# Optimization experiments

Measured on AMD Instinct MI355X. Metric: run time of the kernel, lower is better.

## Reference

```python
import jax, jax.numpy as jnp
import numpy as np
from math import sqrt

B, C1, H1, W1 = 8, 256, 32, 32
C2, H2, W2 = 256, 32, 32
NH, KD, VD = 8, 64, 64


def setup_inputs() -> dict:
    key = jax.random.key(0)
    k = jax.random.split(key, 6)
    s = 0.02
    return {
        "input1": jax.random.normal(k[0], (B, C1, H1, W1), jnp.float32),
        "input2": jax.random.normal(k[1], (B, C2, H2, W2), jnp.float32),
        # torch nn.Linear weights are [out, in]; kept in that layout
        "Wk1": jax.random.normal(k[2], (KD * NH, C1), jnp.float32) * s,
        "Wk2": jax.random.normal(k[3], (KD * NH, C2), jnp.float32) * s,
        "Wv2": jax.random.normal(k[4], (VD * NH, C2), jnp.float32) * s,
        "Wo": jax.random.normal(k[5], (C1, VD * NH), jnp.float32) * s,
    }


def reference(input1, input2, Wk1, Wk2, Wv2, Wo):
    b, c1, h1, w1 = input1.shape
    _, c2, h2, w2 = input2.shape
    s1, s2 = h1 * w1, h2 * w2
    # [B, S, C]
    emb1 = input1.reshape(b, c1, s1).transpose(0, 2, 1)
    emb2 = input2.reshape(b, c2, s2).transpose(0, 2, 1)
    # projections -> [B, heads, S, d]
    k1 = (emb1 @ Wk1.T).reshape(b, s1, NH, KD).transpose(0, 2, 1, 3)
    k2 = (emb2 @ Wk2.T).reshape(b, s2, NH, KD).transpose(0, 2, 1, 3)
    v2 = (emb2 @ Wv2.T).reshape(b, s2, NH, VD).transpose(0, 2, 1, 3)
    # attention: [B, heads, S1, S2]
    scores = jnp.einsum("bhqd,bhkd->bhqk", k1, k2) / sqrt(KD)
    attn = jax.nn.softmax(scores, axis=-1)
    attn = jnp.nan_to_num(attn, nan=0.0)
    out = jnp.einsum("bhqk,bhkd->bhqd", attn, v2)  # [B, heads, S1, VD]
    out = out.transpose(0, 2, 1, 3).reshape(b, s1, NH * VD)
    out = out @ Wo.T  # [B, S1, C1]
    return out.transpose(0, 2, 1).reshape(b, c1, h1, w1)
```

## Files before the change

kernel.cpp:

```cpp
#include <hip/hip_runtime.h>
#include <stdint.h>

typedef __bf16 bf16_t;
typedef __attribute__((ext_vector_type(8))) __bf16 bf16x8;
typedef __attribute__((ext_vector_type(4))) __bf16 bf16x4;
typedef __attribute__((ext_vector_type(4))) float f32x4;

#define NB 8
#define NC 256
#define NS 1024
#define NHD 8
#define ND 64
#define NO 512

#define QK_SCALE 0.18033688011112042f

__device__ __forceinline__ f32x4 mfma16(bf16x8 a, bf16x8 b, f32x4 c) {
  return __builtin_amdgcn_mfma_f32_16x16x32_bf16(a, b, c, 0, 0, 0);
}

__device__ __forceinline__ void gll16(const bf16_t* g, const bf16_t* l) {
  auto gp = (const __attribute__((address_space(1))) void*)(uintptr_t)g;
  auto lp = (__attribute__((address_space(3))) void*)(uint32_t)(uintptr_t)l;
  __builtin_amdgcn_global_load_lds(gp, lp, 16, 0, 0);
}

__global__ __launch_bounds__(256) void k_tcvt(const float* __restrict__ x,
                                              bf16_t* __restrict__ xt) {
  __shared__ float tile[32][33];
  int b = blockIdx.z;
  int s0 = blockIdx.x * 32, c0 = blockIdx.y * 32;
  int tx = threadIdx.x, ty = threadIdx.y;
  const float* xb = x + (size_t)b * NC * NS;
#pragma unroll
  for (int i = 0; i < 4; ++i)
    tile[ty + 8 * i][tx] = xb[(size_t)(c0 + ty + 8 * i) * NS + s0 + tx];
  __syncthreads();
  bf16_t* xtb = xt + (size_t)b * NS * NC;
#pragma unroll
  for (int i = 0; i < 4; ++i)
    xtb[(size_t)(s0 + ty + 8 * i) * NC + c0 + tx] =
        (bf16_t)tile[tx][ty + 8 * i];
}

__global__ __launch_bounds__(256) void k_cvt4(
    const float* __restrict__ s0, const float* __restrict__ s1,
    const float* __restrict__ s2, const float* __restrict__ s3,
    bf16_t* __restrict__ d0, bf16_t* __restrict__ d1,
    bf16_t* __restrict__ d2, bf16_t* __restrict__ d3) {
  const float* s;
  bf16_t* d;
  switch (blockIdx.y) {
    case 0: s = s0; d = d0; break;
    case 1: s = s1; d = d1; break;
    case 2: s = s2; d = d2; break;
    default: s = s3; d = d3; break;
  }
  int i = (blockIdx.x * 256 + threadIdx.x) * 4;
  float4 v = *reinterpret_cast<const float4*>(s + i);
  bf16x4 o;
  o[0] = (bf16_t)v.x; o[1] = (bf16_t)v.y;
  o[2] = (bf16_t)v.z; o[3] = (bf16_t)v.w;
  *reinterpret_cast<bf16x4*>(d + i) = o;
}

__global__ __launch_bounds__(256) void k_projKs(const bf16_t* __restrict__ W,
                                                const bf16_t* __restrict__ XT,
                                                bf16_t* __restrict__ K,
                                                float scale) {
  __shared__ __align__(16) bf16_t lw[2][128 * 128];
  __shared__ __align__(16) bf16_t lx[2][128 * 128];
  int id = blockIdx.x;
  int b = id & 7;
  int ob = ((id >> 3) & 3) * 128;
  int sb = (id >> 5) * 128;
  int tid = threadIdx.x, wid = tid >> 6, lane = tid & 63;
  int lr = lane & 15, g = lane >> 4;
  const bf16_t* wsrc = W + (size_t)ob * NC;
  const bf16_t* xsrc = XT + ((size_t)b * NS + sb) * NC;

  int sr = tid >> 4, sc = tid & 15;
#pragma unroll
  for (int h = 0; h < 2; ++h)
#pragma unroll
    for (int it = 0; it < 8; ++it) {
      int row = it * 16 + sr;
      int cs = (sc & 8) | ((sc & 7) ^ (row & 7));
      gll16(wsrc + (size_t)row * NC + h * 128 + cs * 8,
            &lw[h][(it * 16 + wid * 4) * 128]);
      gll16(xsrc + (size_t)row * NC + h * 128 + cs * 8,
            &lx[h][(it * 16 + wid * 4) * 128]);
    }

  int o0 = (wid >> 1) * 64, s0 = (wid & 1) * 64;
  f32x4 acc[4][4];
#pragma unroll
  for (int mt = 0; mt < 4; ++mt)
#pragma unroll
    for (int nt = 0; nt < 4; ++nt) acc[mt][nt] = (f32x4){0.f, 0.f, 0.f, 0.f};

  asm volatile("s_waitcnt vmcnt(16)" ::: "memory");
  __builtin_amdgcn_s_barrier();
#pragma unroll
  for (int h = 0; h < 2; ++h) {
    if (h == 1) {
      asm volatile("s_waitcnt vmcnt(0)" ::: "memory");
      __builtin_amdgcn_s_barrier();
    }
#pragma unroll
    for (int kk = 0; kk < 4; ++kk) {
      int j = kk * 4 + g;
      bf16x8 av[4], bv[4];
#pragma unroll
      for (int mt = 0; mt < 4; ++mt) {
        int row = o0 + mt * 16 + lr;
        int jj = (j & 8) | ((j & 7) ^ (row & 7));
        av[mt] = *reinterpret_cast<const bf16x8*>(&lw[h][row * 128 + jj * 8]);
      }
#pragma unroll
      for (int nt = 0; nt < 4; ++nt) {
        int row = s0 + nt * 16 + lr;
        int jj = (j & 8) | ((j & 7) ^ (row & 7));
        bv[nt] = *reinterpret_cast<const bf16x8*>(&lx[h][row * 128 + jj * 8]);
      }
#pragma unroll
      for (int mt = 0; mt < 4; ++mt)
#pragma unroll
        for (int nt = 0; nt < 4; ++nt)
          acc[mt][nt] = mfma16(av[mt], bv[nt], acc[mt][nt]);
    }
  }
#pragma unroll
  for (int mt = 0; mt < 4; ++mt) {
    int oRow = ob + o0 + mt * 16 + g * 4;
    int hh = oRow >> 6, d0 = oRow & 63;
#pragma unroll
    for (int nt = 0; nt < 4; ++nt) {
      int s = sb + s0 + nt * 16 + lr;
      bf16x4 pk;
      pk[0] = (bf16_t)(acc[mt][nt][0] * scale);
      pk[1] = (bf16_t)(acc[mt][nt][1] * scale);
      pk[2] = (bf16_t)(acc[mt][nt][2] * scale);
      pk[3] = (bf16_t)(acc[mt][nt][3] * scale);
      *reinterpret_cast<bf16x4*>(
          K + (((size_t)b * NHD + hh) * NS + s) * ND + d0) = pk;
    }
  }
}

__global__ __launch_bounds__(256) void k_projVs(const bf16_t* __restrict__ Wv,
                                                const bf16_t* __restrict__ XT,
                                                bf16_t* __restrict__ VT) {
  __shared__ __align__(16) bf16_t lw[2][128 * 128];
  __shared__ __align__(16) bf16_t lx[2][128 * 128];
  int id = blockIdx.x;
  int b = id & 7;
  int ob = ((id >> 3) & 3) * 128;
  int sb = (id >> 5) * 128;
  int tid = threadIdx.x, wid = tid >> 6, lane = tid & 63;
  int lr = lane & 15, g = lane >> 4;
  const bf16_t* wsrc = Wv + (size_t)ob * NC;
  const bf16_t* xsrc = XT + ((size_t)b * NS + sb) * NC;

  int sr = tid >> 4, sc = tid & 15;
#pragma unroll
  for (int h = 0; h < 2; ++h)
#pragma unroll
    for (int it = 0; it < 8; ++it) {
      int row = it * 16 + sr;
      int cs = (sc & 8) | ((sc & 7) ^ (row & 7));
      gll16(wsrc + (size_t)row * NC + h * 128 + cs * 8,
            &lw[h][(it * 16 + wid * 4) * 128]);
      gll16(xsrc + (size_t)row * NC + h * 128 + cs * 8,
            &lx[h][(it * 16 + wid * 4) * 128]);
    }

  int s0 = (wid >> 1) * 64, o0 = (wid & 1) * 64;
  f32x4 acc[4][4];
#pragma unroll
  for (int mt = 0; mt < 4; ++mt)
#pragma unroll
    for (int nt = 0; nt < 4; ++nt) acc[mt][nt] = (f32x4){0.f, 0.f, 0.f, 0.f};

  asm volatile("s_waitcnt vmcnt(16)" ::: "memory");
  __builtin_amdgcn_s_barrier();
#pragma unroll
  for (int h = 0; h < 2; ++h) {
    if (h == 1) {
      asm volatile("s_waitcnt vmcnt(0)" ::: "memory");
      __builtin_amdgcn_s_barrier();
    }
#pragma unroll
    for (int kk = 0; kk < 4; ++kk) {
      int j = kk * 4 + g;
      bf16x8 av[4], bv[4];
#pragma unroll
      for (int mt = 0; mt < 4; ++mt) {
        int row = s0 + mt * 16 + lr;
        int jj = (j & 8) | ((j & 7) ^ (row & 7));
        av[mt] = *reinterpret_cast<const bf16x8*>(&lx[h][row * 128 + jj * 8]);
      }
#pragma unroll
      for (int nt = 0; nt < 4; ++nt) {
        int row = o0 + nt * 16 + lr;
        int jj = (j & 8) | ((j & 7) ^ (row & 7));
        bv[nt] = *reinterpret_cast<const bf16x8*>(&lw[h][row * 128 + jj * 8]);
      }
#pragma unroll
      for (int mt = 0; mt < 4; ++mt)
#pragma unroll
        for (int nt = 0; nt < 4; ++nt)
          acc[mt][nt] = mfma16(av[mt], bv[nt], acc[mt][nt]);
    }
  }
#pragma unroll
  for (int mt = 0; mt < 4; ++mt) {
    int sRow = sb + s0 + mt * 16 + g * 4;
#pragma unroll
    for (int nt = 0; nt < 4; ++nt) {
      int o = ob + o0 + nt * 16 + lr;
      int hh = o >> 6, d = o & 63;
      bf16x4 pk;
      pk[0] = (bf16_t)acc[mt][nt][0];
      pk[1] = (bf16_t)acc[mt][nt][1];
      pk[2] = (bf16_t)acc[mt][nt][2];
      pk[3] = (bf16_t)acc[mt][nt][3];
      *reinterpret_cast<bf16x4*>(
          VT + (((size_t)b * NHD + hh) * ND + d) * NS + sRow) = pk;
    }
  }
}

__global__ __launch_bounds__(256) void k_attn(const bf16_t* __restrict__ K1,
                                              const bf16_t* __restrict__ K2,
                                              const bf16_t* __restrict__ VT,
                                              bf16_t* __restrict__ AO) {
  __shared__ __align__(16) bf16_t kbuf[2][64 * 64];
  __shared__ __align__(16) bf16_t vbuf[2][64 * 64];
  __shared__ __align__(16) bf16_t plds[4][32 * 64];

  int id = blockIdx.x;
  int bh = (id & 7) * 8 + ((id >> 3) & 7);
  int qb = (id >> 6) * 128;
  int tid = threadIdx.x, wid = tid >> 6, lane = tid & 63;
  int lr = lane & 15, g = lane >> 4;
  const bf16_t* k1 = K1 + (size_t)bh * NS * ND;
  const bf16_t* k2 = K2 + (size_t)bh * NS * ND;
  const bf16_t* vt = VT + (size_t)bh * ND * NS;
  int q0 = qb + wid * 32;

  bf16x8 aq[2][2];
#pragma unroll
  for (int qg = 0; qg < 2; ++qg)
#pragma unroll
    for (int kh = 0; kh < 2; ++kh)
      aq[qg][kh] = *reinterpret_cast<const bf16x8*>(
          k1 + (size_t)(q0 + qg * 16 + lr) * ND + kh * 32 + g * 8);

  f32x4 acc[2][4];
  float l[2][4];
#pragma unroll
  for (int qg = 0; qg < 2; ++qg)
#pragma unroll
    for (int j = 0; j < 4; ++j) {
      acc[qg][j] = (f32x4){0.f, 0.f, 0.f, 0.f};
      l[qg][j] = 0.f;
    }

  int srow = lane >> 3;
  int sx = ((lane & 7) ^ srow) * 8;
  auto stage = [&](int kc, int bs) {
#pragma unroll
    for (int i2 = 0; i2 < 2; ++i2) {
      int rb = (wid * 2 + i2) * 8;
      int row = rb + srow;
      gll16(k2 + (size_t)(kc + row) * ND + sx, &kbuf[bs][(wid * 2 + i2) * 512]);
      gll16(vt + (size_t)row * NS + kc + sx, &vbuf[bs][(wid * 2 + i2) * 512]);
    }
  };

  stage(0, 0);

  bf16_t* pw = plds[wid];
  int swzr = (lr & 7) << 3;
  for (int it = 0; it < 16; ++it) {
    int cur = it & 1;
    if (it < 15) {
      stage((it + 1) * 64, cur ^ 1);
      asm volatile("s_waitcnt vmcnt(4)" ::: "memory");
    } else {
      asm volatile("s_waitcnt vmcnt(0)" ::: "memory");
    }
    __builtin_amdgcn_s_barrier();
    const bf16_t* kb = kbuf[cur];
    const bf16_t* vb = vbuf[cur];

    f32x4 sc[2][4];
#pragma unroll
    for (int qg = 0; qg < 2; ++qg)
#pragma unroll
      for (int t = 0; t < 4; ++t) sc[qg][t] = (f32x4){0.f, 0.f, 0.f, 0.f};
#pragma unroll
    for (int t = 0; t < 4; ++t) {
      const bf16_t* kr = kb + (t * 16 + lr) * 64;
      bf16x8 b0 = *reinterpret_cast<const bf16x8*>(kr + ((g ^ (lr & 7)) << 3));
      bf16x8 b1 =
          *reinterpret_cast<const bf16x8*>(kr + (((4 + g) ^ (lr & 7)) << 3));
#pragma unroll
      for (int qg = 0; qg < 2; ++qg) {
        sc[qg][t] = mfma16(aq[qg][0], b0, sc[qg][t]);
        sc[qg][t] = mfma16(aq[qg][1], b1, sc[qg][t]);
      }
    }
#pragma unroll
    for (int qg = 0; qg < 2; ++qg)
#pragma unroll
      for (int r = 0; r < 4; ++r) {
        float p0 = __builtin_amdgcn_exp2f(sc[qg][0][r]);
        float p1 = __builtin_amdgcn_exp2f(sc[qg][1][r]);
        float p2 = __builtin_amdgcn_exp2f(sc[qg][2][r]);
        float p3 = __builtin_amdgcn_exp2f(sc[qg][3][r]);
        l[qg][r] += (p0 + p1) + (p2 + p3);
        int q = qg * 16 + g * 4 + r;
        int swz = (q & 7) << 3;
        pw[q * 64 + ((0 * 16 + lr) ^ swz)] = (bf16_t)p0;
        pw[q * 64 + ((1 * 16 + lr) ^ swz)] = (bf16_t)p1;
        pw[q * 64 + ((2 * 16 + lr) ^ swz)] = (bf16_t)p2;
        pw[q * 64 + ((3 * 16 + lr) ^ swz)] = (bf16_t)p3;
      }
#pragma unroll
    for (int kc2 = 0; kc2 < 2; ++kc2) {
      bf16x8 pA[2];
#pragma unroll
      for (int qg = 0; qg < 2; ++qg)
        pA[qg] = *reinterpret_cast<const bf16x8*>(
            pw + (qg * 16 + lr) * 64 + ((kc2 * 32 + g * 8) ^ swzr));
#pragma unroll
      for (int dt = 0; dt < 4; ++dt) {
        const bf16_t* vr = vb + (dt * 16 + lr) * 64;
        bf16x8 vB = *reinterpret_cast<const bf16x8*>(
            vr + (((kc2 * 4 + g) ^ (lr & 7)) << 3));
#pragma unroll
        for (int qg = 0; qg < 2; ++qg)
          acc[qg][dt] = mfma16(pA[qg], vB, acc[qg][dt]);
      }
    }
    __builtin_amdgcn_s_barrier();
  }

  int b = bh >> 3, h = bh & 7;
#pragma unroll
  for (int qg = 0; qg < 2; ++qg) {
    float linv[4];
#pragma unroll
    for (int r = 0; r < 4; ++r) {
      float rs = l[qg][r];
      rs += __shfl_xor(rs, 1);
      rs += __shfl_xor(rs, 2);
      rs += __shfl_xor(rs, 4);
      rs += __shfl_xor(rs, 8);
      linv[r] = 1.0f / rs;
    }
#pragma unroll
    for (int dt = 0; dt < 4; ++dt) {
      int d = dt * 16 + lr;
#pragma unroll
      for (int r = 0; r < 4; ++r) {
        int s = q0 + qg * 16 + g * 4 + r;
        AO[((size_t)b * NS + s) * NO + h * ND + d] =
            (bf16_t)(acc[qg][dt][r] * linv[r]);
      }
    }
  }
}

__global__ __launch_bounds__(256) void k_oprojs(const bf16_t* __restrict__ Wob,
                                                const bf16_t* __restrict__ AO,
                                                float* __restrict__ OUT) {
  __shared__ __align__(16) bf16_t la[64 * 512];
  __shared__ __align__(16) bf16_t lb[2][128 * 128];
  int id = blockIdx.x;
  int b = id & 7;
  int cb = ((id >> 3) & 3) * 64;
  int sb = (id >> 5) * 128;
  int tid = threadIdx.x, wid = tid >> 6, lane = tid & 63;
  int lr = lane & 15, g = lane >> 4;
  const bf16_t* asrc = Wob + (size_t)cb * NO;
  const bf16_t* bsrc = AO + ((size_t)b * NS + sb) * NO;

  {
    int c = lane;
#pragma unroll
    for (int it = 0; it < 16; ++it) {
      int row = it * 4 + wid;
      int cs = (c & 56) | ((c & 7) ^ (row & 7));
      gll16(asrc + (size_t)row * NO + cs * 8, &la[row * 512]);
    }
  }
  int sr = tid >> 4, sc = tid & 15;
  auto stageB = [&](int ch) {
#pragma unroll
    for (int it = 0; it < 8; ++it) {
      int row = it * 16 + sr;
      int cs = (sc & 8) | ((sc & 7) ^ (row & 7));
      gll16(bsrc + (size_t)row * NO + ch * 128 + cs * 8,
            &lb[ch & 1][(it * 16 + wid * 4) * 128]);
    }
  };
  stageB(0);
  stageB(1);
  asm volatile("s_waitcnt vmcnt(8)" ::: "memory");
  __builtin_amdgcn_s_barrier();

  int c0 = (wid >> 1) * 32, s0 = (wid & 1) * 64;
  f32x4 acc[2][4];
#pragma unroll
  for (int mt = 0; mt < 2; ++mt)
#pragma unroll
    for (int nt = 0; nt < 4; ++nt) acc[mt][nt] = (f32x4){0.f, 0.f, 0.f, 0.f};

#pragma unroll
  for (int ch = 0; ch < 4; ++ch) {
#pragma unroll
    for (int kk = 0; kk < 4; ++kk) {
      int j = kk * 4 + g;
      bf16x8 av[2], bv[4];
#pragma unroll
      for (int mt = 0; mt < 2; ++mt) {
        int row = c0 + mt * 16 + lr;
        int jh = ch * 16 + j;
        int jj = (jh & 56) | ((jh & 7) ^ (row & 7));
        av[mt] = *reinterpret_cast<const bf16x8*>(&la[row * 512 + jj * 8]);
      }
#pragma unroll
      for (int nt = 0; nt < 4; ++nt) {
        int row = s0 + nt * 16 + lr;
        int jj = (j & 8) | ((j & 7) ^ (row & 7));
        bv[nt] =
            *reinterpret_cast<const bf16x8*>(&lb[ch & 1][row * 128 + jj * 8]);
      }
#pragma unroll
      for (int mt = 0; mt < 2; ++mt)
#pragma unroll
        for (int nt = 0; nt < 4; ++nt)
          acc[mt][nt] = mfma16(av[mt], bv[nt], acc[mt][nt]);
    }
    if (ch < 3) {
      __builtin_amdgcn_s_barrier();
      if (ch + 2 < 4) {
        stageB(ch + 2);
        asm volatile("s_waitcnt vmcnt(8)" ::: "memory");
      } else {
        asm volatile("s_waitcnt vmcnt(0)" ::: "memory");
      }
      __builtin_amdgcn_s_barrier();
    }
  }
#pragma unroll
  for (int mt = 0; mt < 2; ++mt) {
    int c = cb + c0 + mt * 16 + g * 4;
#pragma unroll
    for (int nt = 0; nt < 4; ++nt) {
      int s = sb + s0 + nt * 16 + lr;
#pragma unroll
      for (int r = 0; r < 4; ++r)
        OUT[((size_t)b * NC + c + r) * NS + s] = acc[mt][nt][r];
    }
  }
}

extern "C" void kernel_launch(void* const* d_in, const int* in_sizes, int n_in,
                              void* d_out, int out_size, void* d_ws,
                              size_t ws_size, hipStream_t stream) {
  const float* in1 = (const float*)d_in[0];
  const float* in2 = (const float*)d_in[1];
  const float* Wk1 = (const float*)d_in[2];
  const float* Wk2 = (const float*)d_in[3];
  const float* Wv2 = (const float*)d_in[4];
  const float* Wo = (const float*)d_in[5];
  float* out = (float*)d_out;

  bf16_t* w = (bf16_t*)d_ws;
  bf16_t* XT1 = w;
  bf16_t* XT2 = XT1 + (size_t)NB * NS * NC;
  bf16_t* K1 = XT2 + (size_t)NB * NS * NC;
  bf16_t* K2 = K1 + (size_t)NB * NHD * NS * ND;
  bf16_t* VT = K2 + (size_t)NB * NHD * NS * ND;
  bf16_t* AO = VT + (size_t)NB * NHD * NS * ND;
  bf16_t* Wk1b = AO + (size_t)NB * NS * NO;
  bf16_t* Wk2b = Wk1b + NO * NC;
  bf16_t* Wv2b = Wk2b + NO * NC;
  bf16_t* Wob = Wv2b + NO * NC;

  dim3 tb(32, 8);
  k_tcvt<<<dim3(NS / 32, NC / 32, NB), tb, 0, stream>>>(in1, XT1);
  k_tcvt<<<dim3(NS / 32, NC / 32, NB), tb, 0, stream>>>(in2, XT2);
  k_cvt4<<<dim3(128, 4), 256, 0, stream>>>(Wk1, Wk2, Wv2, Wo, Wk1b, Wk2b,
                                           Wv2b, Wob);

  k_projKs<<<256, 256, 0, stream>>>(Wk1b, XT1, K1, QK_SCALE);
  k_projKs<<<256, 256, 0, stream>>>(Wk2b, XT2, K2, 1.0f);
  k_projVs<<<256, 256, 0, stream>>>(Wv2b, XT2, VT);

  k_attn<<<512, 256, 0, stream>>>(K1, K2, VT, AO);

  k_oprojs<<<256, 256, 0, stream>>>(Wob, AO, out);
}
```

Baseline: 72.23 us.

## Merge prep and projection launches, pipeline projection K-loop, transpose score MFMA

Merges the two transpose-convert kernels and the weight-convert kernel into one prep launch. The three projection GEMMs become a single 768-block launch that uses 64-wide K chunks, double-buffered LDS staging and a smaller LDS footprint, which should allow more blocks per CU. In attention, the score MFMA is transposed so each lane holds four consecutive keys and writes P as packed bf16x4 stores, and the row-sum reduction now takes fewer shuffles. The intent is to cut launch overhead and improve load/compute overlap and occupancy, at the cost of more selector branching inside the kernels.

```diff
diff --git a/kernel.cpp b/kernel.cpp
--- a/kernel.cpp
+++ b/kernel.cpp
@@ -25,103 +25,115 @@
   __builtin_amdgcn_global_load_lds(gp, lp, 16, 0, 0);
 }
 
-__global__ __launch_bounds__(256) void k_tcvt(const float* __restrict__ x,
-                                              bf16_t* __restrict__ xt) {
-  __shared__ float tile[32][33];
-  int b = blockIdx.z;
-  int s0 = blockIdx.x * 32, c0 = blockIdx.y * 32;
+__global__ __launch_bounds__(256) void k_prep(
+    const float* __restrict__ in1, const float* __restrict__ in2,
+    const float* __restrict__ w0, const float* __restrict__ w1,
+    const float* __restrict__ w2, const float* __restrict__ w3,
+    bf16_t* __restrict__ xt1, bf16_t* __restrict__ xt2,
+    bf16_t* __restrict__ wb0, bf16_t* __restrict__ wb1,
+    bf16_t* __restrict__ wb2, bf16_t* __restrict__ wb3) {
+  int z = blockIdx.z;
   int tx = threadIdx.x, ty = threadIdx.y;
-  const float* xb = x + (size_t)b * NC * NS;
-#pragma unroll
-  for (int i = 0; i < 4; ++i)
-    tile[ty + 8 * i][tx] = xb[(size_t)(c0 + ty + 8 * i) * NS + s0 + tx];
-  __syncthreads();
-  bf16_t* xtb = xt + (size_t)b * NS * NC;
-#pragma unroll
-  for (int i = 0; i < 4; ++i)
-    xtb[(size_t)(s0 + ty + 8 * i) * NC + c0 + tx] =
-        (bf16_t)tile[tx][ty + 8 * i];
-}
-
-__global__ __launch_bounds__(256) void k_cvt4(
-    const float* __restrict__ s0, const float* __restrict__ s1,
-    const float* __restrict__ s2, const float* __restrict__ s3,
-    bf16_t* __restrict__ d0, bf16_t* __restrict__ d1,
-    bf16_t* __restrict__ d2, bf16_t* __restrict__ d3) {
-  const float* s;
-  bf16_t* d;
-  switch (blockIdx.y) {
-    case 0: s = s0; d = d0; break;
-    case 1: s = s1; d = d1; break;
-    case 2: s = s2; d = d2; break;
-    default: s = s3; d = d3; break;
-  }
-  int i = (blockIdx.x * 256 + threadIdx.x) * 4;
-  float4 v = *reinterpret_cast<const float4*>(s + i);
-  bf16x4 o;
-  o[0] = (bf16_t)v.x; o[1] = (bf16_t)v.y;
-  o[2] = (bf16_t)v.z; o[3] = (bf16_t)v.w;
-  *reinterpret_cast<bf16x4*>(d + i) = o;
-}
-
-__global__ __launch_bounds__(256) void k_projKs(const bf16_t* __restrict__ W,
-                                                const bf16_t* __restrict__ XT,
-                                                bf16_t* __restrict__ K,
-                                                float scale) {
-  __shared__ __align__(16) bf16_t lw[2][128 * 128];
-  __shared__ __align__(16) bf16_t lx[2][128 * 128];
+  if (z < 16) {
+    __shared__ float tile[32][33];
+    const float* x = (z < 8) ? in1 : in2;
+    bf16_t* xt = (z < 8) ? xt1 : xt2;
+    int b = z & 7;
+    int s0 = blockIdx.x * 32, c0 = blockIdx.y * 32;
+    const float* xb = x + (size_t)b * NC * NS;
+#pragma unroll
+    for (int i = 0; i < 4; ++i)
+      tile[ty + 8 * i][tx] = xb[(size_t)(c0 + ty + 8 * i) * NS + s0 + tx];
+    __syncthreads();
+    bf16_t* xtb = xt + (size_t)b * NS * NC;
+#pragma unroll
+    for (int i = 0; i < 4; ++i)
+      xtb[(size_t)(s0 + ty + 8 * i) * NC + c0 + tx] =
+          (bf16_t)tile[tx][ty + 8 * i];
+  } else {
+    int f = ((blockIdx.y * 32 + blockIdx.x) * 256 + ty * 32 + tx) * 4;
+    int mat = f >> 17, off = f & 131071;
+    const float* s;
+    bf16_t* d;
+    if (z == 16) {
+      s = mat ? w1 : w0; d = mat ? wb1 : wb0;
+    } else {
+      s = mat ? w3 : w2; d = mat ? wb3 : wb2;
+    }
+    float4 v = *reinterpret_cast<const float4*>(s + off);
+    bf16x4 o;
+    o[0] = (bf16_t)v.x; o[1] = (bf16_t)v.y;
+    o[2] = (bf16_t)v.z; o[3] = (bf16_t)v.w;
+    *reinterpret_cast<bf16x4*>(d + off) = o;
+  }
+}
+
+__global__ __launch_bounds__(256) void k_proj(
+    const bf16_t* __restrict__ Wk1b, const bf16_t* __restrict__ Wk2b,
+    const bf16_t* __restrict__ Wv2b, const bf16_t* __restrict__ XT1,
+    const bf16_t* __restrict__ XT2, bf16_t* __restrict__ K1,
+    bf16_t* __restrict__ K2, bf16_t* __restrict__ VT) {
+  __shared__ __align__(16) bf16_t lw[2][128 * 64];
+  __shared__ __align__(16) bf16_t lx[2][128 * 64];
   int id = blockIdx.x;
+  int sel = id >> 8;
+  id &= 255;
   int b = id & 7;
   int ob = ((id >> 3) & 3) * 128;
   int sb = (id >> 5) * 128;
   int tid = threadIdx.x, wid = tid >> 6, lane = tid & 63;
   int lr = lane & 15, g = lane >> 4;
+  const bf16_t* W = sel == 0 ? Wk1b : (sel == 1 ? Wk2b : Wv2b);
+  const bf16_t* xt = (sel == 0 ? XT1 : XT2) + ((size_t)b * NS + sb) * NC;
   const bf16_t* wsrc = W + (size_t)ob * NC;
-  const bf16_t* xsrc = XT + ((size_t)b * NS + sb) * NC;
-
-  int sr = tid >> 4, sc = tid & 15;
-#pragma unroll
-  for (int h = 0; h < 2; ++h)
-#pragma unroll
-    for (int it = 0; it < 8; ++it) {
-      int row = it * 16 + sr;
-      int cs = (sc & 8) | ((sc & 7) ^ (row & 7));
-      gll16(wsrc + (size_t)row * NC + h * 128 + cs * 8,
-            &lw[h][(it * 16 + wid * 4) * 128]);
-      gll16(xsrc + (size_t)row * NC + h * 128 + cs * 8,
-            &lx[h][(it * 16 + wid * 4) * 128]);
-    }
-
-  int o0 = (wid >> 1) * 64, s0 = (wid & 1) * 64;
+
+  int srow8 = lane >> 3, scol = lane & 7;
+  auto stage = [&](int c, int bs) {
+#pragma unroll
+    for (int i = 0; i < 4; ++i) {
+      int row = i * 32 + wid * 8 + srow8;
+      int cs = scol ^ (row & 7);
+      gll16(wsrc + (size_t)row * NC + c * 64 + cs * 8,
+            &lw[bs][(i * 32 + wid * 8) * 64]);
+      gll16(xt + (size_t)row * NC + c * 64 + cs * 8,
+            &lx[bs][(i * 32 + wid * 8) * 64]);
+    }
+  };
+  stage(0, 0);
+
+  int m0 = (wid >> 1) * 64, n0 = (wid & 1) * 64;
   f32x4 acc[4][4];
 #pragma unroll
   for (int mt = 0; mt < 4; ++mt)
 #pragma unroll
     for (int nt = 0; nt < 4; ++nt) acc[mt][nt] = (f32x4){0.f, 0.f, 0.f, 0.f};
 
-  asm volatile("s_waitcnt vmcnt(16)" ::: "memory");
-  __builtin_amdgcn_s_barrier();
-#pragma unroll
-  for (int h = 0; h < 2; ++h) {
-    if (h == 1) {
+  for (int c = 0; c < 4; ++c) {
+    int cb2 = c & 1;
+    if (c < 3) {
+      stage(c + 1, cb2 ^ 1);
+      asm volatile("s_waitcnt vmcnt(8)" ::: "memory");
+    } else {
       asm volatile("s_waitcnt vmcnt(0)" ::: "memory");
-      __builtin_amdgcn_s_barrier();
-    }
-#pragma unroll
-    for (int kk = 0; kk < 4; ++kk) {
+    }
+    __builtin_amdgcn_s_barrier();
+    const bf16_t* aw = sel < 2 ? lw[cb2] : lx[cb2];
+    const bf16_t* bx = sel < 2 ? lx[cb2] : lw[cb2];
+#pragma unroll
+    for (int kk = 0; kk < 2; ++kk) {
       int j = kk * 4 + g;
       bf16x8 av[4], bv[4];
 #pragma unroll
       for (int mt = 0; mt < 4; ++mt) {
-        int row = o0 + mt * 16 + lr;
-        int jj = (j & 8) | ((j & 7) ^ (row & 7));
-        av[mt] = *reinterpret_cast<const bf16x8*>(&lw[h][row * 128 + jj * 8]);
+        int row = m0 + mt * 16 + lr;
+        av[mt] =
+            *reinterpret_cast<const bf16x8*>(aw + row * 64 + (j ^ (row & 7)) * 8);
       }
 #pragma unroll
       for (int nt = 0; nt < 4; ++nt) {
-        int row = s0 + nt * 16 + lr;
-        int jj = (j & 8) | ((j & 7) ^ (row & 7));
-        bv[nt] = *reinterpret_cast<const bf16x8*>(&lx[h][row * 128 + jj * 8]);
+        int row = n0 + nt * 16 + lr;
+        bv[nt] =
+            *reinterpret_cast<const bf16x8*>(bx + row * 64 + (j ^ (row & 7)) * 8);
       }
 #pragma unroll
       for (int mt = 0; mt < 4; ++mt)
@@ -129,104 +141,44 @@
         for (int nt = 0; nt < 4; ++nt)
           acc[mt][nt] = mfma16(av[mt], bv[nt], acc[mt][nt]);
     }
-  }
-#pragma unroll
-  for (int mt = 0; mt < 4; ++mt) {
-    int oRow = ob + o0 + mt * 16 + g * 4;
-    int hh = oRow >> 6, d0 = oRow & 63;
-#pragma unroll
-    for (int nt = 0; nt < 4; ++nt) {
-      int s = sb + s0 + nt * 16 + lr;
-      bf16x4 pk;
-      pk[0] = (bf16_t)(acc[mt][nt][0] * scale);
-      pk[1] = (bf16_t)(acc[mt][nt][1] * scale);
-      pk[2] = (bf16_t)(acc[mt][nt][2] * scale);
-      pk[3] = (bf16_t)(acc[mt][nt][3] * scale);
-      *reinterpret_cast<bf16x4*>(
-          K + (((size_t)b * NHD + hh) * NS + s) * ND + d0) = pk;
-    }
-  }
-}
-
-__global__ __launch_bounds__(256) void k_projVs(const bf16_t* __restrict__ Wv,
-                                                const bf16_t* __restrict__ XT,
-                                                bf16_t* __restrict__ VT) {
-  __shared__ __align__(16) bf16_t lw[2][128 * 128];
-  __shared__ __align__(16) bf16_t lx[2][128 * 128];
-  int id = blockIdx.x;
-  int b = id & 7;
-  int ob = ((id >> 3) & 3) * 128;
-  int sb = (id >> 5) * 128;
-  int tid = threadIdx.x, wid = tid >> 6, lane = tid & 63;
-  int lr = lane & 15, g = lane >> 4;
-  const bf16_t* wsrc = Wv + (size_t)ob * NC;
-  const bf16_t* xsrc = XT + ((size_t)b * NS + sb) * NC;
-
-  int sr = tid >> 4, sc = tid & 15;
-#pragma unroll
-  for (int h = 0; h < 2; ++h)
-#pragma unroll
-    for (int it = 0; it < 8; ++it) {
-      int row = it * 16 + sr;
-      int cs = (sc & 8) | ((sc & 7) ^ (row & 7));
-      gll16(wsrc + (size_t)row * NC + h * 128 + cs * 8,
-            &lw[h][(it * 16 + wid * 4) * 128]);
-      gll16(xsrc + (size_t)row * NC + h * 128 + cs * 8,
-            &lx[h][(it * 16 + wid * 4) * 128]);
-    }
-
-  int s0 = (wid >> 1) * 64, o0 = (wid & 1) * 64;
-  f32x4 acc[4][4];
-#pragma unroll
-  for (int mt = 0; mt < 4; ++mt)
-#pragma unroll
-    for (int nt = 0; nt < 4; ++nt) acc[mt][nt] = (f32x4){0.f, 0.f, 0.f, 0.f};
-
-  asm volatile("s_waitcnt vmcnt(16)" ::: "memory");
-  __builtin_amdgcn_s_barrier();
-#pragma unroll
-  for (int h = 0; h < 2; ++h) {
-    if (h == 1) {
-      asm volatile("s_waitcnt vmcnt(0)" ::: "memory");
-      __builtin_amdgcn_s_barrier();
-    }
-#pragma unroll
-    for (int kk = 0; kk < 4; ++kk) {
-      int j = kk * 4 + g;
-      bf16x8 av[4], bv[4];
-#pragma unroll
-      for (int mt = 0; mt < 4; ++mt) {
-        int row = s0 + mt * 16 + lr;
-        int jj = (j & 8) | ((j & 7) ^ (row & 7));
-        av[mt] = *reinterpret_cast<const bf16x8*>(&lx[h][row * 128 + jj * 8]);
-      }
+    __builtin_amdgcn_s_barrier();
+  }
+
+  if (sel < 2) {
+    float scale = sel == 0 ? QK_SCALE : 1.0f;
+    bf16_t* K = sel == 0 ? K1 : K2;
+#pragma unroll
+    for (int mt = 0; mt < 4; ++mt) {
+      int oRow = ob + m0 + mt * 16 + g * 4;
+      int hh = oRow >> 6, d0 = oRow & 63;
 #pragma unroll
       for (int nt = 0; nt < 4; ++nt) {
-        int row = o0 + nt * 16 + lr;
-        int jj = (j & 8) | ((j & 7) ^ (row & 7));
-        bv[nt] = *reinterpret_cast<const bf16x8*>(&lw[h][row * 128 + jj * 8]);
-      }
-#pragma unroll
-      for (int mt = 0; mt < 4; ++mt)
-#pragma unroll
-        for (int nt = 0; nt < 4; ++nt)
-          acc[mt][nt] = mfma16(av[mt], bv[nt], acc[mt][nt]);
-    }
-  }
-#pragma unroll
-  for (int mt = 0; mt < 4; ++mt) {
-    int sRow = sb + s0 + mt * 16 + g * 4;
-#pragma unroll
-    for (int nt = 0; nt < 4; ++nt) {
-      int o = ob + o0 + nt * 16 + lr;
-      int hh = o >> 6, d = o & 63;
-      bf16x4 pk;
-      pk[0] = (bf16_t)acc[mt][nt][0];
-      pk[1] = (bf16_t)acc[mt][nt][1];
-      pk[2] = (bf16_t)acc[mt][nt][2];
-      pk[3] = (bf16_t)acc[mt][nt][3];
-      *reinterpret_cast<bf16x4*>(
-          VT + (((size_t)b * NHD + hh) * ND + d) * NS + sRow) = pk;
+        int s = sb + n0 + nt * 16 + lr;
+        bf16x4 pk;
+        pk[0] = (bf16_t)(acc[mt][nt][0] * scale);
+        pk[1] = (bf16_t)(acc[mt][nt][1] * scale);
+        pk[2] = (bf16_t)(acc[mt][nt][2] * scale);
+        pk[3] = (bf16_t)(acc[mt][nt][3] * scale);
+        *reinterpret_cast<bf16x4*>(
+            K + (((size_t)b * NHD + hh) * NS + s) * ND + d0) = pk;
+      }
+    }
+  } else {
+#pragma unroll
+    for (int mt = 0; mt < 4; ++mt) {
+      int sRow = sb + m0 + mt * 16 + g * 4;
+#pragma unroll
+      for (int nt = 0; nt < 4; ++nt) {
+        int o = ob + n0 + nt * 16 + lr;
+        int hh = o >> 6, d = o & 63;
+        bf16x4 pk;
+        pk[0] = (bf16_t)acc[mt][nt][0];
+        pk[1] = (bf16_t)acc[mt][nt][1];
+        pk[2] = (bf16_t)acc[mt][nt][2];
+        pk[3] = (bf16_t)acc[mt][nt][3];
+        *reinterpret_cast<bf16x4*>(
+            VT + (((size_t)b * NHD + hh) * ND + d) * NS + sRow) = pk;
+      }
     }
   }
 }
@@ -258,31 +210,26 @@
           k1 + (size_t)(q0 + qg * 16 + lr) * ND + kh * 32 + g * 8);
 
   f32x4 acc[2][4];
-  float l[2][4];
+  float l[2] = {0.f, 0.f};
 #pragma unroll
   for (int qg = 0; qg < 2; ++qg)
 #pragma unroll
-    for (int j = 0; j < 4; ++j) {
-      acc[qg][j] = (f32x4){0.f, 0.f, 0.f, 0.f};
-      l[qg][j] = 0.f;
-    }
+    for (int dt = 0; dt < 4; ++dt) acc[qg][dt] = (f32x4){0.f, 0.f, 0.f, 0.f};
 
   int srow = lane >> 3;
   int sx = ((lane & 7) ^ srow) * 8;
   auto stage = [&](int kc, int bs) {
 #pragma unroll
     for (int i2 = 0; i2 < 2; ++i2) {
-      int rb = (wid * 2 + i2) * 8;
-      int row = rb + srow;
+      int row = (wid * 2 + i2) * 8 + srow;
       gll16(k2 + (size_t)(kc + row) * ND + sx, &kbuf[bs][(wid * 2 + i2) * 512]);
       gll16(vt + (size_t)row * NS + kc + sx, &vbuf[bs][(wid * 2 + i2) * 512]);
     }
   };
-
   stage(0, 0);
 
   bf16_t* pw = plds[wid];
-  int swzr = (lr & 7) << 3;
+  int keyr = lr & 14;
   for (int it = 0; it < 16; ++it) {
     int cur = it & 1;
     if (it < 15) {
@@ -295,11 +242,11 @@
     const bf16_t* kb = kbuf[cur];
     const bf16_t* vb = vbuf[cur];
 
-    f32x4 sc[2][4];
+    f32x4 sct[2][4];
 #pragma unroll
     for (int qg = 0; qg < 2; ++qg)
 #pragma unroll
-      for (int t = 0; t < 4; ++t) sc[qg][t] = (f32x4){0.f, 0.f, 0.f, 0.f};
+      for (int t = 0; t < 4; ++t) sct[qg][t] = (f32x4){0.f, 0.f, 0.f, 0.f};
 #pragma unroll
     for (int t = 0; t < 4; ++t) {
       const bf16_t* kr = kb + (t * 16 + lr) * 64;
@@ -308,25 +255,24 @@
           *reinterpret_cast<const bf16x8*>(kr + (((4 + g) ^ (lr & 7)) << 3));
 #pragma unroll
       for (int qg = 0; qg < 2; ++qg) {
-        sc[qg][t] = mfma16(aq[qg][0], b0, sc[qg][t]);
-        sc[qg][t] = mfma16(aq[qg][1], b1, sc[qg][t]);
+        sct[qg][t] = mfma16(b0, aq[qg][0], sct[qg][t]);
+        sct[qg][t] = mfma16(b1, aq[qg][1], sct[qg][t]);
       }
     }
 #pragma unroll
     for (int qg = 0; qg < 2; ++qg)
 #pragma unroll
-      for (int r = 0; r < 4; ++r) {
-        float p0 = __builtin_amdgcn_exp2f(sc[qg][0][r]);
-        float p1 = __builtin_amdgcn_exp2f(sc[qg][1][r]);
-        float p2 = __builtin_amdgcn_exp2f(sc[qg][2][r]);
-        float p3 = __builtin_amdgcn_exp2f(sc[qg][3][r]);
-        l[qg][r] += (p0 + p1) + (p2 + p3);
-        int q = qg * 16 + g * 4 + r;
-        int swz = (q & 7) << 3;
-        pw[q * 64 + ((0 * 16 + lr) ^ swz)] = (bf16_t)p0;
-        pw[q * 64 + ((1 * 16 + lr) ^ swz)] = (bf16_t)p1;
-        pw[q * 64 + ((2 * 16 + lr) ^ swz)] = (bf16_t)p2;
-        pw[q * 64 + ((3 * 16 + lr) ^ swz)] = (bf16_t)p3;
+      for (int t = 0; t < 4; ++t) {
+        float p0 = __builtin_amdgcn_exp2f(sct[qg][t][0]);
+        float p1 = __builtin_amdgcn_exp2f(sct[qg][t][1]);
+        float p2 = __builtin_amdgcn_exp2f(sct[qg][t][2]);
+        float p3 = __builtin_amdgcn_exp2f(sct[qg][t][3]);
+        l[qg] += (p0 + p1) + (p2 + p3);
+        bf16x4 pk;
+        pk[0] = (bf16_t)p0; pk[1] = (bf16_t)p1;
+        pk[2] = (bf16_t)p2; pk[3] = (bf16_t)p3;
+        int c8 = (t * 4 + g) ^ keyr;
+        *reinterpret_cast<bf16x4*>(pw + (qg * 16 + lr) * 64 + c8 * 4) = pk;
       }
 #pragma unroll
     for (int kc2 = 0; kc2 < 2; ++kc2) {
@@ -334,7 +280,7 @@
 #pragma unroll
       for (int qg = 0; qg < 2; ++qg)
         pA[qg] = *reinterpret_cast<const bf16x8*>(
-            pw + (qg * 16 + lr) * 64 + ((kc2 * 32 + g * 8) ^ swzr));
+            pw + (qg * 16 + lr) * 64 + ((kc2 * 8 + g * 2) ^ keyr) * 4);
 #pragma unroll
       for (int dt = 0; dt < 4; ++dt) {
         const bf16_t* vr = vb + (dt * 16 + lr) * 64;
@@ -349,18 +295,20 @@
   }
 
   int b = bh >> 3, h = bh & 7;
+  float L[2];
+#pragma unroll
+  for (int qg = 0; qg < 2; ++qg) {
+    float rs = l[qg];
+    rs += __shfl_xor(rs, 16);
+    rs += __shfl_xor(rs, 32);
+    L[qg] = rs;
+  }
 #pragma unroll
   for (int qg = 0; qg < 2; ++qg) {
     float linv[4];
 #pragma unroll
-    for (int r = 0; r < 4; ++r) {
-      float rs = l[qg][r];
-      rs += __shfl_xor(rs, 1);
-      rs += __shfl_xor(rs, 2);
-      rs += __shfl_xor(rs, 4);
-      rs += __shfl_xor(rs, 8);
-      linv[r] = 1.0f / rs;
-    }
+    for (int r = 0; r < 4; ++r)
+      linv[r] = 1.0f / __shfl(L[qg], g * 4 + r);
 #pragma unroll
     for (int dt = 0; dt < 4; ++dt) {
       int d = dt * 16 + lr;
@@ -492,15 +440,10 @@
   bf16_t* Wv2b = Wk2b + NO * NC;
   bf16_t* Wob = Wv2b + NO * NC;
 
-  dim3 tb(32, 8);
-  k_tcvt<<<dim3(NS / 32, NC / 32, NB), tb, 0, stream>>>(in1, XT1);
-  k_tcvt<<<dim3(NS / 32, NC / 32, NB), tb, 0, stream>>>(in2, XT2);
-  k_cvt4<<<dim3(128, 4), 256, 0, stream>>>(Wk1, Wk2, Wv2, Wo, Wk1b, Wk2b,
-                                           Wv2b, Wob);
-
-  k_projKs<<<256, 256, 0, stream>>>(Wk1b, XT1, K1, QK_SCALE);
-  k_projKs<<<256, 256, 0, stream>>>(Wk2b, XT2, K2, 1.0f);
-  k_projVs<<<256, 256, 0, stream>>>(Wv2b, XT2, VT);
+  k_prep<<<dim3(32, 8, 18), dim3(32, 8), 0, stream>>>(
+      in1, in2, Wk1, Wk2, Wv2, Wo, XT1, XT2, Wk1b, Wk2b, Wv2b, Wob);
+
+  k_proj<<<768, 256, 0, stream>>>(Wk1b, Wk2b, Wv2b, XT1, XT2, K1, K2, VT);
 
   k_attn<<<512, 256, 0, stream>>>(K1, K2, VT, AO);
 
```

Measured after the change: 59.34 us, median of 4. -17.8%, faster.
